# Optimization experiments

Measured on AMD Instinct MI355X. Metric: run time of the kernel, lower is better.

The kernel has to match this reference:

```python
import jax, jax.numpy as jnp
import numpy as np

EPS = 1e-06
N_HEADS = 8


def setup_inputs() -> dict:
    key = jax.random.key(0)
    ks = jax.random.split(key, 9)
    B, M, T, C = 2, 64, 256, 512
    s = 0.02
    return {
        "x": jax.random.normal(ks[0], (B, M, T, C), dtype=jnp.float32),
        "Wq": jax.random.normal(ks[1], (C, C), dtype=jnp.float32) * s,
        "bq": jnp.zeros((C,), dtype=jnp.float32),
        "Wk": jax.random.normal(ks[2], (C, C), dtype=jnp.float32) * s,
        "bk": jnp.zeros((C,), dtype=jnp.float32),
        "Wv": jax.random.normal(ks[3], (C, C), dtype=jnp.float32) * s,
        "bv": jnp.zeros((C,), dtype=jnp.float32),
        "Wp": jax.random.normal(ks[4], (C, C), dtype=jnp.float32) * s,
        "bp": jnp.zeros((C,), dtype=jnp.float32),
    }


def _proj_heads(x, W, b, N, D):
    # nn.Linear: x @ W.T + b, then view(B,M,T,N,D).transpose(2,3) -> [B,M,N,T,D]
    B, M, T, C = x.shape
    y = jnp.einsum('bmtc,dc->bmtd', x, W) + b
    return y.reshape(B, M, T, N, D).transpose(0, 1, 3, 2, 4)


def reference(x, Wq, bq, Wk, bk, Wv, bv, Wp, bp):
    B, M, T, C = x.shape
    N = N_HEADS
    D = C // N
    q = _proj_heads(x, Wq, bq, N, D)  # [B,M,N,T,D]
    k = _proj_heads(x, Wk, bk, N, D)
    v = _proj_heads(x, Wv, bv, N, D)
    # ELU+1 feature map
    q = jax.nn.elu(q) + 1.0
    k = jax.nn.elu(k) + 1.0
    # KtV = k^T @ v : [B,M,N,D,D]
    KtV = jnp.einsum('bmntd,bmnte->bmnde', k, v)
    # Z = 1 / (q @ sum_t k + eps) : [B,M,N,T]
    ksum = jnp.sum(k, axis=-2)  # [B,M,N,D]
    z = 1.0 / (jnp.einsum('bmntd,bmnd->bmnt', q, ksum) + EPS)
    # Original does Z.expand(...,D) @ KtV; since Z is constant over the D axis,
    # this equals z[t] * sum_d KtV[d, e] -- compute that directly (faithful math).
    KtV_colsum = jnp.sum(KtV, axis=-2)  # [B,M,N,D]
    V = z[..., None] * KtV_colsum[..., None, :]  # [B,M,N,T,D]
    V = V.transpose(0, 1, 3, 2, 4).reshape(B, M, T, N * D)
    out = jnp.einsum('bmtc,dc->bmtd', V, Wp) + bp
    return out
```

## Files before the change

### kernel.cpp

```cpp
#include <hip/hip_runtime.h>
#include <hip/hip_bf16.h>

#define BM_ 128
#define T_  256
#define C_  512
#define NH  8
#define DH  64

typedef __bf16 bf16;
typedef __attribute__((ext_vector_type(8))) __bf16 bf16x8;
typedef __attribute__((ext_vector_type(4))) float f32x4;

__device__ __forceinline__ float elu1(float v){ return v > 0.f ? v + 1.f : __expf(v); }

__device__ __forceinline__ unsigned short f2bf(float f){
  unsigned u = __float_as_uint(f);
  u += 0x7fffu + ((u >> 16) & 1u);
  return (unsigned short)(u >> 16);
}

__device__ __forceinline__ float bf2f(unsigned short b){
  return __uint_as_float(((unsigned)b) << 16);
}

__device__ __forceinline__ unsigned cvtpk(float lo, float hi){
  unsigned r;
  asm("v_cvt_pk_bf16_f32 %0, %1, %2" : "=v"(r) : "v"(lo), "v"(hi));
  return r;
}

#define GLOAD16(gptr, lptr) __builtin_amdgcn_global_load_lds( \
  (const __attribute__((address_space(1))) void*)(gptr), \
  (__attribute__((address_space(3))) void*)(lptr), 16, 0, 0)

#define FENCE() asm volatile("" ::: "memory")

__global__ __launch_bounds__(256) void wcvt_kernel(
    const float* __restrict__ wk, const float* __restrict__ wq,
    unsigned short* __restrict__ ok, unsigned short* __restrict__ oq)
{
  int i = blockIdx.x * 256 + threadIdx.x;
  float4 v = reinterpret_cast<const float4*>(wk)[i];
  ushort4 o;
  o.x = f2bf(v.x); o.y = f2bf(v.y); o.z = f2bf(v.z); o.w = f2bf(v.w);
  reinterpret_cast<ushort4*>(ok)[i] = o;
  v = reinterpret_cast<const float4*>(wq)[i];
  o.x = f2bf(v.x); o.y = f2bf(v.y); o.z = f2bf(v.z); o.w = f2bf(v.w);
  reinterpret_cast<ushort4*>(oq)[i] = o;
}

template<int MODE>
__global__ __launch_bounds__(512, 2) void gemm_proj(
    const bf16* __restrict__ A, const float* __restrict__ Axf,
    unsigned short* __restrict__ xbout,
    const bf16* __restrict__ Bw, const float* __restrict__ bias,
    float* __restrict__ krow, float* __restrict__ ksum2,
    const float* __restrict__ ksum2_in, float* __restrict__ zden)
{
  __shared__ bf16 As[2][256 * 64];
  __shared__ bf16 Bs[2][256 * 64];

  const int tid  = threadIdx.x;
  const int lane = tid & 63;
  const int wid  = tid >> 6;
  const int wr   = wid >> 2, wc = wid & 3;

  const int L  = ((blockIdx.x & 7) << 5) + (blockIdx.x >> 3);
  const int tn = L & 1, tm = L >> 1;

  const bf16* Ab = A  + (size_t)(tm * 256) * C_;
  const bf16* Bb = Bw + (size_t)(tn * 256) * C_;

  const int srow  = tid >> 3;
  const int sslot = tid & 7;
  const int fr = lane & 15, fq = lane >> 4;

  f32x4 acc[8][4];
#pragma unroll
  for (int m = 0; m < 8; ++m)
#pragma unroll
    for (int n = 0; n < 4; ++n) acc[m][n] = (f32x4){0.f, 0.f, 0.f, 0.f};

#define STG(XS, Xb, b, h, kt) do { \
  _Pragma("unroll") \
  for (int q = 0; q < 2; ++q) { \
    int r_ = (h) * 128 + q * 64 + srow; \
    GLOAD16(Xb + (size_t)r_ * C_ + (kt) * 64 + ((sslot ^ (r_ & 7)) << 3), \
            &XS[b][(((h) * 128 + q * 64) << 6) + (tid << 3)]); \
  } } while (0)

#define LOFF(row, sl) (((row) << 6) + ((((sl) ^ ((row) & 7))) << 3))

#define AISSUE(LO, HI, h, kt) do { \
  _Pragma("unroll") \
  for (int q = 0; q < 2; ++q) { \
    int r_ = (h) * 128 + q * 64 + srow; \
    const float* gp = Axf + (size_t)(tm * 256 + r_) * C_ + (kt) * 64 + sslot * 8; \
    LO[q] = *reinterpret_cast<const float4*>(gp); \
    HI[q] = *reinterpret_cast<const float4*>(gp + 4); \
  } } while (0)

#define AWRITE(LO, HI, b, h, kt) do { \
  _Pragma("unroll") \
  for (int q = 0; q < 2; ++q) { \
    int r_ = (h) * 128 + q * 64 + srow; \
    uint4 v; \
    v.x = cvtpk(LO[q].x, LO[q].y); \
    v.y = cvtpk(LO[q].z, LO[q].w); \
    v.z = cvtpk(HI[q].x, HI[q].y); \
    v.w = cvtpk(HI[q].z, HI[q].w); \
    *reinterpret_cast<uint4*>(&As[b][LOFF(r_, sslot)]) = v; \
    if (tn == 0) \
      *reinterpret_cast<uint4*>(xbout + (size_t)(tm * 256 + r_) * C_ + (kt) * 64 + sslot * 8) = v; \
  } } while (0)

  float4 a0l[2], a0h[2], a1l[2], a1h[2];

  if constexpr (MODE == 0) {
    AISSUE(a0l, a0h, 0, 0); AISSUE(a1l, a1h, 1, 0);
    STG(Bs, Bb, 0, 0, 0);   STG(Bs, Bb, 0, 1, 0);
    AWRITE(a0l, a0h, 0, 0, 0); AWRITE(a1l, a1h, 0, 1, 0);
  } else {
    STG(As, Ab, 0, 0, 0); STG(As, Ab, 0, 1, 0);
    STG(Bs, Bb, 0, 0, 0); STG(Bs, Bb, 0, 1, 0);
  }
  asm volatile("s_waitcnt vmcnt(0) lgkmcnt(0)" ::: "memory");
  __builtin_amdgcn_s_barrier();
  FENCE();

  bf16x8 af[4][2], bfr[4][2];

  for (int t = 0; t < 8; ++t) {
    const int cur = t & 1;
    const bool pre = (t < 7);
#pragma unroll
    for (int m = 0; m < 4; ++m)
#pragma unroll
      for (int kk = 0; kk < 2; ++kk) {
        int row = wr * 128 + m * 16 + fr;
        af[m][kk] = *reinterpret_cast<const bf16x8*>(&As[cur][LOFF(row, kk * 4 + fq)]);
      }
#pragma unroll
    for (int n = 0; n < 2; ++n)
#pragma unroll
      for (int kk = 0; kk < 2; ++kk) {
        int row = wc * 64 + n * 16 + fr;
        bfr[n][kk] = *reinterpret_cast<const bf16x8*>(&Bs[cur][LOFF(row, kk * 4 + fq)]);
      }
    if (pre) {
      if constexpr (MODE == 0) AISSUE(a0l, a0h, 0, t + 1);
      else                     STG(As, Ab, cur ^ 1, 0, t + 1);
      STG(Bs, Bb, cur ^ 1, 0, t + 1);
    }
    __builtin_amdgcn_s_setprio(1);
#pragma unroll
    for (int m = 0; m < 4; ++m)
#pragma unroll
      for (int n = 0; n < 2; ++n)
#pragma unroll
        for (int kk = 0; kk < 2; ++kk)
          acc[m][n] = __builtin_amdgcn_mfma_f32_16x16x32_bf16(af[m][kk], bfr[n][kk], acc[m][n], 0, 0, 0);
    __builtin_amdgcn_s_setprio(0);
    __builtin_amdgcn_s_barrier();
    FENCE();
#pragma unroll
    for (int n = 0; n < 2; ++n)
#pragma unroll
      for (int kk = 0; kk < 2; ++kk) {
        int row = wc * 64 + (n + 2) * 16 + fr;
        bfr[n + 2][kk] = *reinterpret_cast<const bf16x8*>(&Bs[cur][LOFF(row, kk * 4 + fq)]);
      }
    if (pre) {
      if constexpr (MODE == 0) AISSUE(a1l, a1h, 1, t + 1);
      else                     STG(As, Ab, cur ^ 1, 1, t + 1);
      STG(Bs, Bb, cur ^ 1, 1, t + 1);
    }
    __builtin_amdgcn_s_setprio(1);
#pragma unroll
    for (int m = 0; m < 4; ++m)
#pragma unroll
      for (int n = 0; n < 2; ++n)
#pragma unroll
        for (int kk = 0; kk < 2; ++kk)
          acc[m][n + 2] = __builtin_amdgcn_mfma_f32_16x16x32_bf16(af[m][kk], bfr[n + 2][kk], acc[m][n + 2], 0, 0, 0);
    __builtin_amdgcn_s_setprio(0);
    __builtin_amdgcn_s_barrier();
    FENCE();
#pragma unroll
    for (int m = 0; m < 4; ++m)
#pragma unroll
      for (int kk = 0; kk < 2; ++kk) {
        int row = wr * 128 + 64 + m * 16 + fr;
        af[m][kk] = *reinterpret_cast<const bf16x8*>(&As[cur][LOFF(row, kk * 4 + fq)]);
      }
    __builtin_amdgcn_s_setprio(1);
#pragma unroll
    for (int m = 0; m < 4; ++m)
#pragma unroll
      for (int n = 0; n < 2; ++n)
#pragma unroll
        for (int kk = 0; kk < 2; ++kk)
          acc[m + 4][n] = __builtin_amdgcn_mfma_f32_16x16x32_bf16(af[m][kk], bfr[n][kk], acc[m + 4][n], 0, 0, 0);
    __builtin_amdgcn_s_setprio(0);
    if (pre) { if constexpr (MODE == 0) AWRITE(a0l, a0h, cur ^ 1, 0, t + 1); }
    __builtin_amdgcn_s_barrier();
    FENCE();
    __builtin_amdgcn_s_setprio(1);
#pragma unroll
    for (int m = 0; m < 4; ++m)
#pragma unroll
      for (int n = 0; n < 2; ++n)
#pragma unroll
        for (int kk = 0; kk < 2; ++kk)
          acc[m + 4][n + 2] = __builtin_amdgcn_mfma_f32_16x16x32_bf16(af[m][kk], bfr[n + 2][kk], acc[m + 4][n + 2], 0, 0, 0);
    __builtin_amdgcn_s_setprio(0);
    if (pre) { if constexpr (MODE == 0) AWRITE(a1l, a1h, cur ^ 1, 1, t + 1); }
    if constexpr (MODE == 0) {
      if (tn == 0) asm volatile("s_waitcnt vmcnt(4) lgkmcnt(0)" ::: "memory");
      else         asm volatile("s_waitcnt vmcnt(0) lgkmcnt(0)" ::: "memory");
    } else {
      asm volatile("s_waitcnt vmcnt(0) lgkmcnt(0)" ::: "memory");
    }
    __builtin_amdgcn_s_barrier();
    FENCE();
  }
#undef STG
#undef LOFF
#undef AISSUE
#undef AWRITE

  const int bm   = tm;
  const int head = tn * 4 + wc;
  float bj[4];
#pragma unroll
  for (int n = 0; n < 4; ++n) bj[n] = bias[tn * 256 + wc * 64 + n * 16 + fr];

  if (MODE == 0) {
    float cs[4] = {0.f, 0.f, 0.f, 0.f};
#pragma unroll
    for (int m = 0; m < 8; ++m) {
#pragma unroll
      for (int r = 0; r < 4; ++r) {
        float rs = 0.f;
#pragma unroll
        for (int n = 0; n < 4; ++n) {
          float v = elu1(acc[m][n][r] + bj[n]);
          rs += v;
          cs[n] += v;
        }
#pragma unroll
        for (int msk = 1; msk < 16; msk <<= 1) rs += __shfl_xor(rs, msk);
        if (fr == 0) {
          int tg = wr * 128 + m * 16 + fq * 4 + r;
          krow[((size_t)bm * NH + head) * T_ + tg] = rs;
        }
      }
    }
#pragma unroll
    for (int n = 0; n < 4; ++n) {
      cs[n] += __shfl_xor(cs[n], 16);
      cs[n] += __shfl_xor(cs[n], 32);
      if (fq == 0)
        ksum2[((size_t)wr * BM_ + bm) * C_ + tn * 256 + wc * 64 + n * 16 + fr] = cs[n];
    }
  } else {
    float ks[4];
#pragma unroll
    for (int n = 0; n < 4; ++n) {
      size_t col = (size_t)bm * C_ + tn * 256 + wc * 64 + n * 16 + fr;
      ks[n] = ksum2_in[col] + ksum2_in[(size_t)BM_ * C_ + col];
    }
#pragma unroll
    for (int m = 0; m < 8; ++m) {
#pragma unroll
      for (int r = 0; r < 4; ++r) {
        float zs = 0.f;
#pragma unroll
        for (int n = 0; n < 4; ++n) zs = fmaf(elu1(acc[m][n][r] + bj[n]), ks[n], zs);
#pragma unroll
        for (int msk = 1; msk < 16; msk <<= 1) zs += __shfl_xor(zs, msk);
        if (fr == 0) {
          int tg = wr * 128 + m * 16 + fq * 4 + r;
          zden[((size_t)bm * NH + head) * T_ + tg] = zs;
        }
      }
    }
  }
}

__global__ __launch_bounds__(256) void xk_kernel(
    const unsigned short* __restrict__ xb, const float* __restrict__ krow,
    float* __restrict__ xk4, float* __restrict__ srow4)
{
  const int bm = blockIdx.x, qt = blockIdx.y, tid = threadIdx.x;
  __shared__ float krs[NH * 64];
#pragma unroll
  for (int p = 0; p < 2; ++p) {
    int idx = tid + p * 256;
    int n = idx >> 6, t = idx & 63;
    krs[idx] = krow[((size_t)bm * NH + n) * T_ + qt * 64 + t];
  }
  __syncthreads();
  float a0[8], a1[8];
#pragma unroll
  for (int n = 0; n < 8; ++n) { a0[n] = 0.f; a1[n] = 0.f; }
  const unsigned short* xp = xb + ((size_t)bm * T_ + qt * 64) * C_ + tid * 2;
  for (int t = 0; t < 64; ++t) {
    ushort2 u = *reinterpret_cast<const ushort2*>(xp + (size_t)t * C_);
    float x0 = bf2f(u.x), x1 = bf2f(u.y);
#pragma unroll
    for (int n = 0; n < 8; ++n) {
      float kr = krs[n * 64 + t];
      a0[n] = fmaf(kr, x0, a0[n]);
      a1[n] = fmaf(kr, x1, a1[n]);
    }
  }
#pragma unroll
  for (int n = 0; n < 8; ++n)
    *reinterpret_cast<float2*>(&xk4[(((size_t)qt * BM_ + bm) * NH + n) * C_ + tid * 2])
        = make_float2(a0[n], a1[n]);
  if (tid < 8) {
    float s = 0.f;
    for (int t = 0; t < 64; ++t) s += krs[tid * 64 + t];
    srow4[((size_t)qt * BM_ + bm) * NH + tid] = s;
  }
}

__global__ __launch_bounds__(256) void colsum_kernel(
    const float* __restrict__ xk4, const float* __restrict__ srow4,
    const float* __restrict__ Wv, const float* __restrict__ bv,
    float* __restrict__ cs_g)
{
  const int bm0 = blockIdx.x * 8, h = blockIdx.y, tid = threadIdx.x;
  __shared__ float4 xs4[8][128];
#pragma unroll
  for (int p = 0; p < 4; ++p) {
    int idx = tid + p * 256;
    int bmr = idx >> 7, c4 = idx & 127;
    float4 s = make_float4(0.f, 0.f, 0.f, 0.f);
#pragma unroll
    for (int q = 0; q < 4; ++q) {
      float4 u = *reinterpret_cast<const float4*>(
          xk4 + (((size_t)q * BM_ + bm0 + bmr) * NH + h) * C_ + c4 * 4);
      s.x += u.x; s.y += u.y; s.z += u.z; s.w += u.w;
    }
    xs4[bmr][c4] = s;
  }
  __syncthreads();
  const int e = tid & 63, bs = tid >> 6;
  const float4* wv4 = reinterpret_cast<const float4*>(Wv + (size_t)(h * DH + e) * C_);
  float acc0 = 0.f, acc1 = 0.f;
#pragma unroll 4
  for (int c4 = 0; c4 < 128; ++c4) {
    float4 w = wv4[c4];
    float4 a = xs4[bs * 2][c4];
    float4 b = xs4[bs * 2 + 1][c4];
    acc0 += w.x * a.x + w.y * a.y + w.z * a.z + w.w * a.w;
    acc1 += w.x * b.x + w.y * b.y + w.z * b.z + w.w * b.w;
  }
  float bve = bv[h * DH + e];
  int bmA = bm0 + bs * 2, bmB = bmA + 1;
  float sA = 0.f, sB = 0.f;
#pragma unroll
  for (int q = 0; q < 4; ++q) {
    sA += srow4[((size_t)q * BM_ + bmA) * NH + h];
    sB += srow4[((size_t)q * BM_ + bmB) * NH + h];
  }
  cs_g[((size_t)bmA * NH + h) * DH + e] = acc0 + sA * bve;
  cs_g[((size_t)bmB * NH + h) * DH + e] = acc1 + sB * bve;
}

__global__ __launch_bounds__(256) void wbuf_kernel(
    const float* __restrict__ cs_g, const float* __restrict__ Wp,
    float* __restrict__ wbuf)
{
  const int cpt = blockIdx.x, h = blockIdx.y, bm0 = blockIdx.z * 16;
  const int tid = threadIdx.x;
  __shared__ float4 csL4[16][16];
  {
    int bmr = tid >> 4, e4 = tid & 15;
    csL4[bmr][e4] = *reinterpret_cast<const float4*>(
        cs_g + ((size_t)(bm0 + bmr) * NH + h) * DH + e4 * 4);
  }
  __syncthreads();
  const int cp = cpt * 256 + tid;
  float4 wp[16];
  const float4* wpr = reinterpret_cast<const float4*>(Wp + (size_t)cp * C_ + h * DH);
#pragma unroll
  for (int e4 = 0; e4 < 16; ++e4) wp[e4] = wpr[e4];
#pragma unroll
  for (int bmr = 0; bmr < 16; ++bmr) {
    float acc = 0.f;
#pragma unroll
    for (int e4 = 0; e4 < 16; ++e4) {
      float4 c = csL4[bmr][e4];
      acc += wp[e4].x * c.x + wp[e4].y * c.y + wp[e4].z * c.z + wp[e4].w * c.w;
    }
    wbuf[((size_t)(bm0 + bmr) * NH + h) * C_ + cp] = acc;
  }
}

__global__ __launch_bounds__(256) void out_kernel(
    const float* __restrict__ zden, const float* __restrict__ wbuf,
    const float* __restrict__ bp, float* __restrict__ out)
{
  const int bm = blockIdx.x, tt = blockIdx.y, tid = threadIdx.x;
  __shared__ float zs[NH][64];
#pragma unroll
  for (int p = 0; p < 2; ++p) {
    int idx = tid + p * 256;
    int n = idx >> 6, t = idx & 63;
    zs[n][t] = 1.f / (zden[((size_t)bm * NH + n) * T_ + tt * 64 + t] + 1e-6f);
  }
  float2 wv[8];
  const int c2 = tid * 2;
#pragma unroll
  for (int n = 0; n < 8; ++n)
    wv[n] = *reinterpret_cast<const float2*>(wbuf + ((size_t)bm * NH + n) * C_ + c2);
  float2 bpv = *reinterpret_cast<const float2*>(bp + c2);
  __syncthreads();
  float* ob = out + ((size_t)bm * T_ + tt * 64) * C_;
  for (int t = 0; t < 64; ++t) {
    float o0 = bpv.x, o1 = bpv.y;
#pragma unroll
    for (int n = 0; n < 8; ++n) { float z = zs[n][t]; o0 = fmaf(z, wv[n].x, o0); o1 = fmaf(z, wv[n].y, o1); }
    *reinterpret_cast<float2*>(ob + (size_t)t * C_ + c2) = make_float2(o0, o1);
  }
}

extern "C" void kernel_launch(void* const* d_in, const int* in_sizes, int n_in,
                              void* d_out, int out_size, void* d_ws, size_t ws_size,
                              hipStream_t stream)
{
  const float* x  = (const float*)d_in[0];
  const float* Wq = (const float*)d_in[1];
  const float* bq = (const float*)d_in[2];
  const float* Wk = (const float*)d_in[3];
  const float* bk = (const float*)d_in[4];
  const float* Wv = (const float*)d_in[5];
  const float* bv = (const float*)d_in[6];
  const float* Wp = (const float*)d_in[7];
  const float* bp = (const float*)d_in[8];
  float* out = (float*)d_out;

  float* ws    = (float*)d_ws;
  float* zden  = ws;
  float* ksum2 = zden + 262144;
  float* krow  = ksum2 + 131072;
  float* srow4 = krow + 262144;
  float* xk4   = srow4 + 4096;
  float* cs    = xk4 + 2097152;
  float* wbuf  = cs + 65536;
  unsigned short* xb  = (unsigned short*)(wbuf + 524288);
  unsigned short* wkb = xb + 16777216;
  unsigned short* wqb = wkb + 262144;

  wcvt_kernel<<<256, 256, 0, stream>>>(Wk, Wq, wkb, wqb);

  gemm_proj<0><<<256, 512, 0, stream>>>(nullptr, x, xb, (const bf16*)wkb, bk,
                                        krow, ksum2, nullptr, nullptr);
  xk_kernel<<<dim3(BM_, 4), 256, 0, stream>>>(xb, krow, xk4, srow4);
  colsum_kernel<<<dim3(16, 8), 256, 0, stream>>>(xk4, srow4, Wv, bv, cs);
  wbuf_kernel<<<dim3(2, 8, 8), 256, 0, stream>>>(cs, Wp, wbuf);
  gemm_proj<1><<<256, 512, 0, stream>>>((const bf16*)xb, nullptr, nullptr,
                                        (const bf16*)wqb, bq,
                                        nullptr, ksum2, ksum2, zden);
  out_kernel<<<dim3(BM_, 4), 256, 0, stream>>>(zden, wbuf, bp, out);
}
```

Before: 114.5 us.

## Split LDS tiles into K-halves and interleave loads with finer-grained waits

Reorganizes the shared-memory tiles of the projection GEMM into two K-halves of 32 columns each, with a 4-slot XOR swizzle. Each of the four MFMA phases now consumes one K-half for half of the M rows. Global prefetches of the next tile are staggered across phases, and partial vmcnt waits replace full drains so loads stay in flight longer. The intent is to cut register pressure from fragment arrays and to overlap memory with compute better. The risk is miscounted vmcnt values, which would cause races, and a new LDS bank-conflict pattern.

```diff
diff --git a/kernel.cpp b/kernel.cpp
--- a/kernel.cpp
+++ b/kernel.cpp
@@ -57,8 +57,8 @@
     float* __restrict__ krow, float* __restrict__ ksum2,
     const float* __restrict__ ksum2_in, float* __restrict__ zden)
 {
-  __shared__ bf16 As[2][256 * 64];
-  __shared__ bf16 Bs[2][256 * 64];
+  __shared__ bf16 As[2][2 * 8192];
+  __shared__ bf16 Bs[2][2 * 8192];
 
   const int tid  = threadIdx.x;
   const int lane = tid & 63;
@@ -70,9 +70,6 @@
 
   const bf16* Ab = A  + (size_t)(tm * 256) * C_;
   const bf16* Bb = Bw + (size_t)(tn * 256) * C_;
-
-  const int srow  = tid >> 3;
-  const int sslot = tid & 7;
   const int fr = lane & 15, fq = lane >> 4;
 
   f32x4 acc[8][4];
@@ -81,150 +78,149 @@
 #pragma unroll
     for (int n = 0; n < 4; ++n) acc[m][n] = (f32x4){0.f, 0.f, 0.f, 0.f};
 
-#define STG(XS, Xb, b, h, kt) do { \
+#define LOFF(kk, row, sl) ((kk) * 8192 + (row) * 32 + (((sl) ^ ((row) & 3)) << 3))
+
+#define STGX(XS, Xb, b, kk, kt) do { \
   _Pragma("unroll") \
-  for (int q = 0; q < 2; ++q) { \
-    int r_ = (h) * 128 + q * 64 + srow; \
-    GLOAD16(Xb + (size_t)r_ * C_ + (kt) * 64 + ((sslot ^ (r_ & 7)) << 3), \
-            &XS[b][(((h) * 128 + q * 64) << 6) + (tid << 3)]); \
+  for (int j = 0; j < 2; ++j) { \
+    int d_ = j * 512 + tid; int r_ = d_ >> 2; int s_ = d_ & 3; \
+    GLOAD16(Xb + (size_t)r_ * C_ + (kt) * 64 + (kk) * 32 + (((s_ ^ (r_ & 3))) << 3), \
+            &XS[b][(kk) * 8192 + j * 4096 + tid * 8]); \
   } } while (0)
 
-#define LOFF(row, sl) (((row) << 6) + ((((sl) ^ ((row) & 7))) << 3))
-
-#define AISSUE(LO, HI, h, kt) do { \
+#define AISSUE(V, kk, kt) do { \
   _Pragma("unroll") \
-  for (int q = 0; q < 2; ++q) { \
-    int r_ = (h) * 128 + q * 64 + srow; \
-    const float* gp = Axf + (size_t)(tm * 256 + r_) * C_ + (kt) * 64 + sslot * 8; \
-    LO[q] = *reinterpret_cast<const float4*>(gp); \
-    HI[q] = *reinterpret_cast<const float4*>(gp + 4); \
+  for (int j = 0; j < 2; ++j) { \
+    int d_ = j * 512 + tid; int r_ = d_ >> 2; int s_ = d_ & 3; \
+    const float* gp = Axf + (size_t)(tm * 256 + r_) * C_ + (kt) * 64 + (kk) * 32 \
+                      + (((s_ ^ (r_ & 3))) << 3); \
+    V[j * 2]     = *reinterpret_cast<const float4*>(gp); \
+    V[j * 2 + 1] = *reinterpret_cast<const float4*>(gp + 4); \
   } } while (0)
 
-#define AWRITE(LO, HI, b, h, kt) do { \
+#define AWRITE(V, b, kk, kt) do { \
   _Pragma("unroll") \
-  for (int q = 0; q < 2; ++q) { \
-    int r_ = (h) * 128 + q * 64 + srow; \
+  for (int j = 0; j < 2; ++j) { \
+    int d_ = j * 512 + tid; int r_ = d_ >> 2; int s_ = d_ & 3; \
     uint4 v; \
-    v.x = cvtpk(LO[q].x, LO[q].y); \
-    v.y = cvtpk(LO[q].z, LO[q].w); \
-    v.z = cvtpk(HI[q].x, HI[q].y); \
-    v.w = cvtpk(HI[q].z, HI[q].w); \
-    *reinterpret_cast<uint4*>(&As[b][LOFF(r_, sslot)]) = v; \
+    v.x = cvtpk(V[j * 2].x,     V[j * 2].y); \
+    v.y = cvtpk(V[j * 2].z,     V[j * 2].w); \
+    v.z = cvtpk(V[j * 2 + 1].x, V[j * 2 + 1].y); \
+    v.w = cvtpk(V[j * 2 + 1].z, V[j * 2 + 1].w); \
+    *reinterpret_cast<uint4*>(&As[b][(kk) * 8192 + d_ * 8]) = v; \
     if (tn == 0) \
-      *reinterpret_cast<uint4*>(xbout + (size_t)(tm * 256 + r_) * C_ + (kt) * 64 + sslot * 8) = v; \
+      *reinterpret_cast<uint4*>(xbout + (size_t)(tm * 256 + r_) * C_ + (kt) * 64 \
+                                + (kk) * 32 + (((s_ ^ (r_ & 3))) << 3)) = v; \
   } } while (0)
 
-  float4 a0l[2], a0h[2], a1l[2], a1h[2];
+  float4 aK0[4], aK1[4];
 
   if constexpr (MODE == 0) {
-    AISSUE(a0l, a0h, 0, 0); AISSUE(a1l, a1h, 1, 0);
-    STG(Bs, Bb, 0, 0, 0);   STG(Bs, Bb, 0, 1, 0);
-    AWRITE(a0l, a0h, 0, 0, 0); AWRITE(a1l, a1h, 0, 1, 0);
+    AISSUE(aK0, 0, 0); AISSUE(aK1, 1, 0);
+    STGX(Bs, Bb, 0, 0, 0); STGX(Bs, Bb, 0, 1, 0);
+    AWRITE(aK0, 0, 0, 0); AWRITE(aK1, 0, 1, 0);
   } else {
-    STG(As, Ab, 0, 0, 0); STG(As, Ab, 0, 1, 0);
-    STG(Bs, Bb, 0, 0, 0); STG(Bs, Bb, 0, 1, 0);
+    STGX(As, Ab, 0, 0, 0); STGX(Bs, Bb, 0, 0, 0);
+    STGX(As, Ab, 0, 1, 0); STGX(Bs, Bb, 0, 1, 0);
   }
   asm volatile("s_waitcnt vmcnt(0) lgkmcnt(0)" ::: "memory");
   __builtin_amdgcn_s_barrier();
   FENCE();
 
-  bf16x8 af[4][2], bfr[4][2];
+  bf16x8 af[4], bfr[4];
 
   for (int t = 0; t < 8; ++t) {
     const int cur = t & 1;
     const bool pre = (t < 7);
-#pragma unroll
-    for (int m = 0; m < 4; ++m)
-#pragma unroll
-      for (int kk = 0; kk < 2; ++kk) {
-        int row = wr * 128 + m * 16 + fr;
-        af[m][kk] = *reinterpret_cast<const bf16x8*>(&As[cur][LOFF(row, kk * 4 + fq)]);
-      }
-#pragma unroll
-    for (int n = 0; n < 2; ++n)
-#pragma unroll
-      for (int kk = 0; kk < 2; ++kk) {
-        int row = wc * 64 + n * 16 + fr;
-        bfr[n][kk] = *reinterpret_cast<const bf16x8*>(&Bs[cur][LOFF(row, kk * 4 + fq)]);
-      }
+
+#pragma unroll
+    for (int m = 0; m < 4; ++m)
+      af[m] = *reinterpret_cast<const bf16x8*>(&As[cur][LOFF(0, wr * 128 + m * 16 + fr, fq)]);
+#pragma unroll
+    for (int n = 0; n < 4; ++n)
+      bfr[n] = *reinterpret_cast<const bf16x8*>(&Bs[cur][LOFF(0, wc * 64 + n * 16 + fr, fq)]);
     if (pre) {
-      if constexpr (MODE == 0) AISSUE(a0l, a0h, 0, t + 1);
-      else                     STG(As, Ab, cur ^ 1, 0, t + 1);
-      STG(Bs, Bb, cur ^ 1, 0, t + 1);
+      if constexpr (MODE == 0) { AISSUE(aK0, 0, t + 1); STGX(Bs, Bb, cur ^ 1, 0, t + 1); }
+      else                     { STGX(As, Ab, cur ^ 1, 0, t + 1); }
     }
     __builtin_amdgcn_s_setprio(1);
 #pragma unroll
     for (int m = 0; m < 4; ++m)
 #pragma unroll
-      for (int n = 0; n < 2; ++n)
-#pragma unroll
-        for (int kk = 0; kk < 2; ++kk)
-          acc[m][n] = __builtin_amdgcn_mfma_f32_16x16x32_bf16(af[m][kk], bfr[n][kk], acc[m][n], 0, 0, 0);
+      for (int n = 0; n < 4; ++n)
+        acc[m][n] = __builtin_amdgcn_mfma_f32_16x16x32_bf16(af[m], bfr[n], acc[m][n], 0, 0, 0);
     __builtin_amdgcn_s_setprio(0);
     __builtin_amdgcn_s_barrier();
     FENCE();
-#pragma unroll
-    for (int n = 0; n < 2; ++n)
-#pragma unroll
-      for (int kk = 0; kk < 2; ++kk) {
-        int row = wc * 64 + (n + 2) * 16 + fr;
-        bfr[n + 2][kk] = *reinterpret_cast<const bf16x8*>(&Bs[cur][LOFF(row, kk * 4 + fq)]);
-      }
+
+#pragma unroll
+    for (int m = 0; m < 4; ++m)
+      af[m] = *reinterpret_cast<const bf16x8*>(&As[cur][LOFF(0, wr * 128 + 64 + m * 16 + fr, fq)]);
     if (pre) {
-      if constexpr (MODE == 0) AISSUE(a1l, a1h, 1, t + 1);
-      else                     STG(As, Ab, cur ^ 1, 1, t + 1);
-      STG(Bs, Bb, cur ^ 1, 1, t + 1);
+      if constexpr (MODE == 0) { AISSUE(aK1, 1, t + 1); STGX(Bs, Bb, cur ^ 1, 1, t + 1); }
+      else                     { STGX(Bs, Bb, cur ^ 1, 0, t + 1); }
     }
     __builtin_amdgcn_s_setprio(1);
 #pragma unroll
     for (int m = 0; m < 4; ++m)
 #pragma unroll
-      for (int n = 0; n < 2; ++n)
-#pragma unroll
-        for (int kk = 0; kk < 2; ++kk)
-          acc[m][n + 2] = __builtin_amdgcn_mfma_f32_16x16x32_bf16(af[m][kk], bfr[n + 2][kk], acc[m][n + 2], 0, 0, 0);
+      for (int n = 0; n < 4; ++n)
+        acc[m + 4][n] = __builtin_amdgcn_mfma_f32_16x16x32_bf16(af[m], bfr[n], acc[m + 4][n], 0, 0, 0);
     __builtin_amdgcn_s_setprio(0);
+    if constexpr (MODE == 0) {
+      if (pre) { if (tn == 0) asm volatile("s_waitcnt vmcnt(16) lgkmcnt(0)" ::: "memory");
+                 else         asm volatile("s_waitcnt vmcnt(12) lgkmcnt(0)" ::: "memory"); }
+      else     { if (tn == 0) asm volatile("s_waitcnt vmcnt(4) lgkmcnt(0)" ::: "memory");
+                 else         asm volatile("s_waitcnt vmcnt(0) lgkmcnt(0)" ::: "memory"); }
+    } else {
+      if (pre) asm volatile("s_waitcnt vmcnt(4) lgkmcnt(0)" ::: "memory");
+      else     asm volatile("s_waitcnt vmcnt(0) lgkmcnt(0)" ::: "memory");
+    }
     __builtin_amdgcn_s_barrier();
     FENCE();
-#pragma unroll
-    for (int m = 0; m < 4; ++m)
-#pragma unroll
-      for (int kk = 0; kk < 2; ++kk) {
-        int row = wr * 128 + 64 + m * 16 + fr;
-        af[m][kk] = *reinterpret_cast<const bf16x8*>(&As[cur][LOFF(row, kk * 4 + fq)]);
-      }
+
+#pragma unroll
+    for (int m = 0; m < 4; ++m)
+      af[m] = *reinterpret_cast<const bf16x8*>(&As[cur][LOFF(1, wr * 128 + m * 16 + fr, fq)]);
+#pragma unroll
+    for (int n = 0; n < 4; ++n)
+      bfr[n] = *reinterpret_cast<const bf16x8*>(&Bs[cur][LOFF(1, wc * 64 + n * 16 + fr, fq)]);
+    if (pre) { if constexpr (MODE == 1) STGX(As, Ab, cur ^ 1, 1, t + 1); }
     __builtin_amdgcn_s_setprio(1);
 #pragma unroll
     for (int m = 0; m < 4; ++m)
 #pragma unroll
-      for (int n = 0; n < 2; ++n)
-#pragma unroll
-        for (int kk = 0; kk < 2; ++kk)
-          acc[m + 4][n] = __builtin_amdgcn_mfma_f32_16x16x32_bf16(af[m][kk], bfr[n][kk], acc[m + 4][n], 0, 0, 0);
+      for (int n = 0; n < 4; ++n)
+        acc[m][n] = __builtin_amdgcn_mfma_f32_16x16x32_bf16(af[m], bfr[n], acc[m][n], 0, 0, 0);
     __builtin_amdgcn_s_setprio(0);
-    if (pre) { if constexpr (MODE == 0) AWRITE(a0l, a0h, cur ^ 1, 0, t + 1); }
+    if (pre) { if constexpr (MODE == 0) AWRITE(aK0, cur ^ 1, 0, t + 1); }
     __builtin_amdgcn_s_barrier();
     FENCE();
+
+#pragma unroll
+    for (int m = 0; m < 4; ++m)
+      af[m] = *reinterpret_cast<const bf16x8*>(&As[cur][LOFF(1, wr * 128 + 64 + m * 16 + fr, fq)]);
+    if (pre) { if constexpr (MODE == 1) STGX(Bs, Bb, cur ^ 1, 1, t + 1); }
     __builtin_amdgcn_s_setprio(1);
 #pragma unroll
     for (int m = 0; m < 4; ++m)
 #pragma unroll
-      for (int n = 0; n < 2; ++n)
-#pragma unroll
-        for (int kk = 0; kk < 2; ++kk)
-          acc[m + 4][n + 2] = __builtin_amdgcn_mfma_f32_16x16x32_bf16(af[m][kk], bfr[n + 2][kk], acc[m + 4][n + 2], 0, 0, 0);
+      for (int n = 0; n < 4; ++n)
+        acc[m + 4][n] = __builtin_amdgcn_mfma_f32_16x16x32_bf16(af[m], bfr[n], acc[m + 4][n], 0, 0, 0);
     __builtin_amdgcn_s_setprio(0);
-    if (pre) { if constexpr (MODE == 0) AWRITE(a1l, a1h, cur ^ 1, 1, t + 1); }
+    if (pre) { if constexpr (MODE == 0) AWRITE(aK1, cur ^ 1, 1, t + 1); }
     if constexpr (MODE == 0) {
-      if (tn == 0) asm volatile("s_waitcnt vmcnt(4) lgkmcnt(0)" ::: "memory");
-      else         asm volatile("s_waitcnt vmcnt(0) lgkmcnt(0)" ::: "memory");
+      if (pre) { if (tn == 0) asm volatile("s_waitcnt vmcnt(10) lgkmcnt(0)" ::: "memory");
+                 else         asm volatile("s_waitcnt vmcnt(6) lgkmcnt(0)" ::: "memory"); }
+      else     {              asm volatile("s_waitcnt vmcnt(0) lgkmcnt(0)" ::: "memory"); }
     } else {
-      asm volatile("s_waitcnt vmcnt(0) lgkmcnt(0)" ::: "memory");
+      if (pre) asm volatile("s_waitcnt vmcnt(4) lgkmcnt(0)" ::: "memory");
+      else     asm volatile("s_waitcnt vmcnt(0) lgkmcnt(0)" ::: "memory");
     }
     __builtin_amdgcn_s_barrier();
     FENCE();
   }
-#undef STG
+#undef STGX
 #undef LOFF
 #undef AISSUE
 #undef AWRITE
```

Result: slower. 119.7 us (+4.6%).
